# Optimization experiments

Measured on AMD Instinct MI355X. Metric: run time of the kernel, lower is better.

## Reference

```python
import jax, jax.numpy as jnp
import numpy as np

D_MODEL = 256
H = 4              # hardcoded in the torch module via repeat(1,4,1)
DIM = D_MODEL // H # 64
N = 4096


def _conv1x1(x, W, b):
    # torch Conv1d(kernel_size=1): [B, Cin, N] -> [B, Cout, N]
    return jnp.einsum('oi,bin->bon', W, x) + b[None, :, None]


def setup_inputs() -> dict:
    key = jax.random.key(0)
    ks = jax.random.split(key, 13)
    s = 0.02
    inp = {
        'query':   jax.random.normal(ks[0], (1, D_MODEL, N), dtype=jnp.float32),
        'key':     jax.random.normal(ks[1], (1, D_MODEL, N), dtype=jnp.float32),
        'value':   jax.random.normal(ks[2], (1, D_MODEL, N), dtype=jnp.float32),
        'coords0': jax.random.normal(ks[3], (1, 3, N), dtype=jnp.float32),
        'coords1': jax.random.normal(ks[4], (1, 3, N), dtype=jnp.float32),
        'Wq': jax.random.normal(ks[5], (D_MODEL, D_MODEL), dtype=jnp.float32) * s,
        'bq': jnp.zeros((D_MODEL,), dtype=jnp.float32),
        'Wk': jax.random.normal(ks[6], (D_MODEL, D_MODEL), dtype=jnp.float32) * s,
        'bk': jnp.zeros((D_MODEL,), dtype=jnp.float32),
        'Wv': jax.random.normal(ks[7], (D_MODEL, D_MODEL), dtype=jnp.float32) * s,
        'bv': jnp.zeros((D_MODEL,), dtype=jnp.float32),
        'Wm': jax.random.normal(ks[8], (D_MODEL + 28, D_MODEL + 28), dtype=jnp.float32) * s,
        'bm': jnp.zeros((D_MODEL + 28,), dtype=jnp.float32),
    }
    return inp


def reference(query, key, value, coords0, coords1, Wq, bq, Wk, bk, Wv, bv, Wm, bm):
    B = query.shape[0]  # must be 1 (hardcoded in original via view(1,4,3,-1))
    Nq = coords0.shape[2]
    Nk = coords1.shape[2]

    # 1x1-conv projections, then split channels into (dim, heads): view(B, dim, H, N)
    q = _conv1x1(query, Wq, bq).reshape(B, DIM, H, Nq)
    k = _conv1x1(key,   Wk, bk).reshape(B, DIM, H, Nk)
    v = _conv1x1(value, Wv, bv).reshape(B, DIM, H, Nk)

    # coords1.repeat(1,4,1).view(1,4,3,-1).transpose(1,2) == broadcast coords over heads
    c1 = jnp.broadcast_to(coords1[:, :, None, :], (B, 3, H, Nk))
    v = jnp.concatenate([v, c1], axis=1)  # [B, DIM+3, H, Nk]

    # attention: scale is query.shape[1]**0.5 == DIM**0.5 (per-head dim)
    scores = jnp.einsum('bdhn,bdhm->bhnm', q, k) / jnp.asarray(DIM, q.dtype) ** 0.5
    prob = jax.nn.softmax(scores, axis=-1)          # [B, H, Nq, Nk]
    x = jnp.einsum('bhnm,bdhm->bdhn', prob, v)      # [B, DIM+3, H, Nq]

    # coordinate augmentation
    c0 = jnp.broadcast_to(coords0[:, :, None, :], (B, 3, H, Nq))
    aug1 = x[:, DIM:DIM + 3] - c0                   # [B, 3, H, Nq]
    aug2 = jnp.linalg.norm(aug1, axis=1, keepdims=True)  # [B, 1, H, Nq]

    y = jnp.concatenate([x, aug1, aug2], axis=1)    # [B, DIM+7, H, Nq]
    y = y.reshape(B, (DIM + 7) * H, Nq)
    return _conv1x1(y, Wm, bm)                      # [B, d_model+28, Nq]
```

## Files before the change

### kernel.cpp

```cpp
#include <hip/hip_runtime.h>
#include <hip/hip_bf16.h>

#define NN 4096

typedef __attribute__((ext_vector_type(8))) short short8;
typedef __attribute__((ext_vector_type(4))) float f32x4;

__device__ __forceinline__ unsigned short f2bf(float f) {
  union { float f; unsigned u; } v; v.f = f;
  unsigned u = v.u;
  u += 0x7fffu + ((u >> 16) & 1u);
  return (unsigned short)(u >> 16);
}

__device__ __forceinline__ unsigned packpair(float a, float b) {
  __hip_bfloat162 h = __float22bfloat162_rn(make_float2(a, b));
  union { __hip_bfloat162 h; unsigned u; } cv; cv.h = h;
  return cv.u;
}

__device__ __forceinline__ float bf2f(unsigned short us) {
  union { unsigned u; float f; } cv; cv.u = (unsigned)us << 16;
  return cv.f;
}

__global__ __launch_bounds__(256) void transpose3_kernel(
    const float* __restrict__ q, const float* __restrict__ k, const float* __restrict__ v,
    unsigned short* __restrict__ Xt, const float* __restrict__ coords1,
    unsigned short* __restrict__ Vb) {
  __shared__ float Tl[64][65];
  const float* X = (blockIdx.z == 0) ? q : (blockIdx.z == 1) ? k : v;
  unsigned short* dst = Xt + (size_t)blockIdx.z * NN * 256;
  const int n0 = blockIdx.x << 6, k0 = blockIdx.y << 6;
  const int t = threadIdx.x;
  const int r = t >> 4, c4 = (t & 15) << 2;
#pragma unroll
  for (int i = 0; i < 4; ++i) {
    const float4 vv = *(const float4*)(X + (size_t)(k0 + r + 16 * i) * NN + n0 + c4);
    Tl[r + 16 * i][c4] = vv.x; Tl[r + 16 * i][c4 + 1] = vv.y;
    Tl[r + 16 * i][c4 + 2] = vv.z; Tl[r + 16 * i][c4 + 3] = vv.w;
  }
  __syncthreads();
  const int kc = (t & 7) << 3;
#pragma unroll
  for (int j = 0; j < 2; ++j) {
    const int n = (t >> 3) + (j << 5);
    unsigned pk[4];
#pragma unroll
    for (int u = 0; u < 4; ++u)
      pk[u] = packpair(Tl[kc + 2 * u][n], Tl[kc + 2 * u + 1][n]);
    *(uint4*)(dst + (size_t)(n0 + n) * 256 + k0 + kc) = *(uint4*)pk;
  }
  if (blockIdx.z == 2 && blockIdx.y == 0) {
    const int rr = t >> 2, seg = t & 3;
    const int h = rr >> 4, d = 64 + (rr & 15);
    unsigned short* vd = Vb + (size_t)(h * 80 + d) * NN + n0 + seg * 16;
    if (d < 67) {
      const float* src = coords1 + (size_t)(d - 64) * NN + n0 + seg * 16;
      unsigned u[8];
#pragma unroll
      for (int i = 0; i < 4; ++i) {
        const float4 cv = *(const float4*)(src + 4 * i);
        u[2 * i] = packpair(cv.x, cv.y);
        u[2 * i + 1] = packpair(cv.z, cv.w);
      }
      *(uint4*)vd = *(uint4*)&u[0];
      *(uint4*)(vd + 8) = *(uint4*)&u[4];
    } else {
      const uint4 zz = make_uint4(0u, 0u, 0u, 0u);
      *(uint4*)vd = zz;
      *(uint4*)(vd + 8) = zz;
    }
  }
}

__global__ __launch_bounds__(256) void proj_gemm_kernel(
    const float* __restrict__ Wq, const float* __restrict__ bq,
    const float* __restrict__ Wk, const float* __restrict__ bk,
    const float* __restrict__ Wv, const float* __restrict__ bv,
    const unsigned short* __restrict__ Xt,
    unsigned short* __restrict__ Qb, unsigned short* __restrict__ Kb,
    unsigned short* __restrict__ Vb) {
  __shared__ __align__(16) unsigned char smem[16384];
  __shared__ float Bls[64];
  const int z = blockIdx.z;
  const float* W  = (z == 0) ? Wq : (z == 1) ? Wk : Wv;
  const float* bb = (z == 0) ? bq : (z == 1) ? bk : bv;
  const unsigned short* Xz = Xt + (size_t)z * NN * 256;
  const int co0 = blockIdx.y << 6;
  const int n0 = blockIdx.x << 6;
  const int tid = threadIdx.x;
  const int w = tid >> 6, l = tid & 63;
  const int wm = w >> 1, wn = w & 1;
  const int c = l & 15, g = l >> 4;
  char* const Al = (char*)smem;
  char* const Bl = (char*)smem + 8192;

  if (tid < 64) Bls[tid] = bb[co0 + tid];

  const int ar = tid >> 2, ac = (tid & 3) << 4;
  const int br = tid >> 3, bch = tid & 7;
  const int aswz = (ar & 7) << 4;
  const int bswz = (br & 7) << 4;

  float4 wa[4];
  uint4 wb[2];
  f32x4 acc[2][2];
#pragma unroll
  for (int mf = 0; mf < 2; ++mf)
#pragma unroll
    for (int nf = 0; nf < 2; ++nf) acc[mf][nf] = (f32x4){0.f, 0.f, 0.f, 0.f};

#define PJ_LOAD(k0_) do { \
  _Pragma("unroll") for (int i = 0; i < 4; ++i) \
    wa[i] = *(const float4*)(W + (size_t)(co0 + ar) * 256 + (k0_) + ac + 4 * i); \
  wb[0] = *(const uint4*)(Xz + (size_t)(n0 + br) * 256 + (k0_) + bch * 8); \
  wb[1] = *(const uint4*)(Xz + (size_t)(n0 + br + 32) * 256 + (k0_) + bch * 8); \
} while (0)

#define PJ_STORE() do { \
  unsigned pk[8]; \
  _Pragma("unroll") for (int i = 0; i < 4; ++i) { \
    pk[2 * i] = packpair(wa[i].x, wa[i].y); \
    pk[2 * i + 1] = packpair(wa[i].z, wa[i].w); \
  } \
  *(uint4*)(Al + ar * 128 + (((ac << 1)) ^ aswz)) = *(uint4*)&pk[0]; \
  *(uint4*)(Al + ar * 128 + (((ac << 1) + 16) ^ aswz)) = *(uint4*)&pk[4]; \
  *(uint4*)(Bl + br * 128 + ((bch << 4) ^ bswz)) = wb[0]; \
  *(uint4*)(Bl + (br + 32) * 128 + ((bch << 4) ^ bswz)) = wb[1]; \
} while (0)

  PJ_LOAD(0);
  PJ_STORE();
  __syncthreads();

  for (int s = 0; s < 4; ++s) {
    const bool hav = (s + 1 < 4);
    if (hav) PJ_LOAD((s + 1) << 6);
    __builtin_amdgcn_s_setprio(1);
#pragma unroll
    for (int ks = 0; ks < 2; ++ks) {
      short8 af[2], bf[2];
#pragma unroll
      for (int mf = 0; mf < 2; ++mf) {
        const int row = wm * 32 + mf * 16 + c;
        af[mf] = *(const short8*)(Al + row * 128 + (((ks << 6) + (g << 4)) ^ ((row & 7) << 4)));
      }
#pragma unroll
      for (int nf = 0; nf < 2; ++nf) {
        const int row = wn * 32 + nf * 16 + c;
        bf[nf] = *(const short8*)(Bl + row * 128 + (((ks << 6) + (g << 4)) ^ ((row & 7) << 4)));
      }
#pragma unroll
      for (int mf = 0; mf < 2; ++mf)
#pragma unroll
        for (int nf = 0; nf < 2; ++nf)
          acc[mf][nf] = __builtin_amdgcn_mfma_f32_16x16x32_bf16(af[mf], bf[nf], acc[mf][nf], 0, 0, 0);
    }
    __builtin_amdgcn_s_setprio(0);
    __syncthreads();
    if (hav) {
      PJ_STORE();
      __syncthreads();
    }
  }

  unsigned short* Clu = (unsigned short*)smem;
  const float scale = (z == 0) ? 0.18033688f : 1.0f;
#pragma unroll
  for (int mf = 0; mf < 2; ++mf)
#pragma unroll
    for (int nf = 0; nf < 2; ++nf)
#pragma unroll
      for (int rr = 0; rr < 4; ++rr) {
        const int row = wm * 32 + mf * 16 + (g << 2) + rr;
        const int col = wn * 32 + nf * 16 + c;
        Clu[row * 72 + col] = f2bf((acc[mf][nf][rr] + Bls[row]) * scale);
      }
  __syncthreads();
  if (z <= 1) {
    unsigned short* Ob = (z == 0) ? Qb : Kb;
    const int d0 = co0 >> 2;
    const int h = tid >> 6, n = tid & 63;
    unsigned u[8];
#pragma unroll
    for (int p = 0; p < 8; ++p)
      u[p] = (unsigned)Clu[((p << 3) + h) * 72 + n] |
             ((unsigned)Clu[((p << 3) + 4 + h) * 72 + n] << 16);
    uint4* dd = (uint4*)(Ob + ((size_t)h * NN + n0 + n) * 64 + d0);
    dd[0] = *(uint4*)&u[0];
    dd[1] = *(uint4*)&u[4];
  } else {
    const int rl = tid >> 2, seg = (tid & 3) << 4;
    const int h = rl & 3, d = (co0 >> 2) + (rl >> 2);
    unsigned short* vd = Vb + (size_t)(h * 80 + d) * NN + n0 + seg;
    *(uint4*)vd = *(const uint4*)((char*)Clu + rl * 144 + (seg << 1));
    *(uint4*)(vd + 8) = *(const uint4*)((char*)Clu + rl * 144 + (seg << 1) + 16);
  }
}

__global__ __launch_bounds__(256, 2) void attn_kernel(
    const unsigned short* __restrict__ Qb, const unsigned short* __restrict__ Kb,
    const unsigned short* __restrict__ Vb, unsigned short* __restrict__ ObT,
    float* __restrict__ Ml, int chunkKeys, int nsplit) {
  __shared__ __align__(16) unsigned char smem[71680];
  const int b = blockIdx.x;
  int x, h, sp;
  if (nsplit >= 2) {
    const int xcd = b & 7, slot = b >> 3;
    const int group = xcd * (nsplit >> 1) + (slot >> 5);
    x = slot & 31; h = group & 3; sp = group >> 2;
  } else {
    x = b & 31; h = (b >> 5) & 3; sp = 0;
  }
  const int qbase = x * 128;
  const int tid = threadIdx.x;
  const int w = tid >> 6;
  const int l = tid & 63;
  const int c = l & 15;
  const int g = l >> 4;
  const int swc = (c & 7) << 4;

  char* const Pls = (char*)smem + 55296 + w * 4096;

  short8 qf[2][2];
#pragma unroll
  for (int qs = 0; qs < 2; ++qs) {
    const unsigned short* qsrc = Qb + (((h * NN) + qbase + w * 32 + qs * 16 + c) << 6) + (g << 3);
    qf[qs][0] = *(const short8*)qsrc;
    qf[qs][1] = *(const short8*)(qsrc + 32);
  }

  f32x4 Of[2][5];
#pragma unroll
  for (int qs = 0; qs < 2; ++qs)
#pragma unroll
    for (int dt = 0; dt < 5; ++dt) Of[qs][dt] = (f32x4){0.f, 0.f, 0.f, 0.f};
  float mrun[2] = {-1e30f, -1e30f};
  float lrun[2] = {0.f, 0.f};

  const int r0 = tid >> 3, ch = tid & 7;
  const int so = (ch << 4) ^ ((r0 & 7) << 4);
  const int mStart = sp * chunkKeys;
  const int niter = chunkKeys >> 6;

  uint4 ska, skb, sva, svb, svc;

#define LOADT(m0_) do { \
    const unsigned short* kbase_ = Kb + ((h * NN + (m0_)) << 6); \
    const unsigned short* vbase_ = Vb + (size_t)(h * 80) * NN + (m0_); \
    ska = *(const uint4*)(kbase_ + (r0 << 6) + (ch << 3)); \
    skb = *(const uint4*)(kbase_ + ((r0 + 32) << 6) + (ch << 3)); \
    sva = *(const uint4*)(vbase_ + (size_t)r0 * NN + (ch << 3)); \
    svb = *(const uint4*)(vbase_ + (size_t)(r0 + 32) * NN + (ch << 3)); \
    if (tid < 128) svc = *(const uint4*)(vbase_ + (size_t)(r0 + 64) * NN + (ch << 3)); \
  } while (0)

#define STORET(bj_) do { \
    char* Kd_ = (char*)smem + (bj_) * 18432; \
    char* Vd_ = Kd_ + 8192; \
    *(uint4*)(Kd_ + r0 * 128 + so) = ska; \
    *(uint4*)(Kd_ + (r0 + 32) * 128 + so) = skb; \
    *(uint4*)(Vd_ + r0 * 128 + so) = sva; \
    *(uint4*)(Vd_ + (r0 + 32) * 128 + so) = svb; \
    if (tid < 128) *(uint4*)(Vd_ + (r0 + 64) * 128 + so) = svc; \
  } while (0)

#define QKSTEP(bj_, DST) do { \
    const char* Kc_ = (char*)smem + (bj_) * 18432; \
    __builtin_amdgcn_s_setprio(1); \
    _Pragma("unroll") for (int t = 0; t < 4; ++t) { \
      const char* rp_ = Kc_ + (t * 16 + c) * 128; \
      const short8 k0_ = *(const short8*)(rp_ + ((g << 4) ^ swc)); \
      const short8 k1_ = *(const short8*)(rp_ + ((64 + (g << 4)) ^ swc)); \
      _Pragma("unroll") for (int qs = 0; qs < 2; ++qs) { \
        f32x4 a_ = (f32x4){0.f, 0.f, 0.f, 0.f}; \
        a_ = __builtin_amdgcn_mfma_f32_16x16x32_bf16(k0_, qf[qs][0], a_, 0, 0, 0); \
        a_ = __builtin_amdgcn_mfma_f32_16x16x32_bf16(k1_, qf[qs][1], a_, 0, 0, 0); \
        DST[qs][t] = a_; \
      } \
    } \
    __builtin_amdgcn_s_setprio(0); \
  } while (0)

#define SMSTEP(SRC) do { \
    _Pragma("unroll") for (int qs = 0; qs < 2; ++qs) { \
      float m01_ = fmaxf(fmaxf(SRC[qs][0][0], SRC[qs][0][1]), fmaxf(SRC[qs][0][2], SRC[qs][0][3])); \
      float m11_ = fmaxf(fmaxf(SRC[qs][1][0], SRC[qs][1][1]), fmaxf(SRC[qs][1][2], SRC[qs][1][3])); \
      float m21_ = fmaxf(fmaxf(SRC[qs][2][0], SRC[qs][2][1]), fmaxf(SRC[qs][2][2], SRC[qs][2][3])); \
      float m31_ = fmaxf(fmaxf(SRC[qs][3][0], SRC[qs][3][1]), fmaxf(SRC[qs][3][2], SRC[qs][3][3])); \
      float mx_ = fmaxf(fmaxf(m01_, m11_), fmaxf(m21_, m31_)); \
      mx_ = fmaxf(mx_, __shfl_xor(mx_, 16)); \
      mx_ = fmaxf(mx_, __shfl_xor(mx_, 32)); \
      if (!__all(mx_ - mrun[qs] <= 11.5f)) { \
        const float mn_ = fmaxf(mrun[qs], mx_); \
        const float a_ = __builtin_amdgcn_exp2f(mrun[qs] - mn_); \
        mrun[qs] = mn_; \
        lrun[qs] *= a_; \
        _Pragma("unroll") for (int dt = 0; dt < 5; ++dt) \
          _Pragma("unroll") for (int r = 0; r < 4; ++r) Of[qs][dt][r] *= a_; \
      } \
      const float mm_ = mrun[qs]; \
      float rs_ = 0.f; \
      unsigned pk_[8]; \
      _Pragma("unroll") for (int t = 0; t < 4; ++t) { \
        const float e0_ = __builtin_amdgcn_exp2f(SRC[qs][t][0] - mm_); \
        const float e1_ = __builtin_amdgcn_exp2f(SRC[qs][t][1] - mm_); \
        const float e2_ = __builtin_amdgcn_exp2f(SRC[qs][t][2] - mm_); \
        const float e3_ = __builtin_amdgcn_exp2f(SRC[qs][t][3] - mm_); \
        rs_ += (e0_ + e1_) + (e2_ + e3_); \
        pk_[t * 2]     = packpair(e0_, e1_); \
        pk_[t * 2 + 1] = packpair(e2_, e3_); \
      } \
      rs_ += __shfl_xor(rs_, 16); \
      rs_ += __shfl_xor(rs_, 32); \
      lrun[qs] += rs_; \
      char* prow_ = Pls + (qs * 16 + c) * 128; \
      _Pragma("unroll") for (int t = 0; t < 4; ++t) \
        *(uint2*)(prow_ + ((t * 32 + (g << 3)) ^ swc)) = make_uint2(pk_[t * 2], pk_[t * 2 + 1]); \
    } \
  } while (0)

#define PVSTEP(bj_) do { \
    short8 pb_[2][2]; \
    _Pragma("unroll") for (int qs = 0; qs < 2; ++qs) { \
      const char* prow_ = Pls + (qs * 16 + c) * 128; \
      pb_[qs][0] = *(const short8*)(prow_ + ((g << 4) ^ swc)); \
      pb_[qs][1] = *(const short8*)(prow_ + ((64 + (g << 4)) ^ swc)); \
    } \
    const char* Vc_ = (char*)smem + (bj_) * 18432 + 8192; \
    __builtin_amdgcn_s_setprio(1); \
    _Pragma("unroll") for (int dt = 0; dt < 5; ++dt) { \
      const char* vp_ = Vc_ + (dt * 16 + c) * 128; \
      const short8 v0_ = *(const short8*)(vp_ + ((g << 4) ^ swc)); \
      const short8 v1_ = *(const short8*)(vp_ + ((64 + (g << 4)) ^ swc)); \
      _Pragma("unroll") for (int qs = 0; qs < 2; ++qs) { \
        Of[qs][dt] = __builtin_amdgcn_mfma_f32_16x16x32_bf16(v0_, pb_[qs][0], Of[qs][dt], 0, 0, 0); \
        Of[qs][dt] = __builtin_amdgcn_mfma_f32_16x16x32_bf16(v1_, pb_[qs][1], Of[qs][dt], 0, 0, 0); \
      } \
    } \
    __builtin_amdgcn_s_setprio(0); \
  } while (0)

  f32x4 sD0[2][4], sD1[2][4];

  LOADT(mStart);
  STORET(0);
  LOADT(mStart + 64);
  __syncthreads();
  QKSTEP(0, sD0);
  STORET(1);
  LOADT(mStart + 128);
  __syncthreads();

  for (int it = 0; it < niter; it += 2) {
    SMSTEP(sD0);
    QKSTEP((it + 1) % 3, sD1);
    PVSTEP(it % 3);
    if (it + 2 < niter) {
      STORET((it + 2) % 3);
      if (it + 3 < niter) LOADT(mStart + ((it + 3) << 6));
    }
    __syncthreads();
    SMSTEP(sD1);
    if (it + 2 < niter) QKSTEP((it + 2) % 3, sD0);
    PVSTEP((it + 1) % 3);
    if (it + 3 < niter) {
      STORET((it + 3) % 3);
      if (it + 4 < niter) LOADT(mStart + ((it + 4) << 6));
    }
    __syncthreads();
  }

#undef LOADT
#undef STORET
#undef QKSTEP
#undef SMSTEP
#undef PVSTEP

  const int hb = sp * 4 + h;
#pragma unroll
  for (int qs = 0; qs < 2; ++qs) {
    const int qg = qbase + w * 32 + qs * 16 + c;
    unsigned short* orow = ObT + ((size_t)hb * NN + qg) * 72;
#pragma unroll
    for (int dt = 0; dt < 5; ++dt) {
      if (dt == 4 && g >= 2) continue;
      const unsigned lo = packpair(Of[qs][dt][0], Of[qs][dt][1]);
      const unsigned hi = packpair(Of[qs][dt][2], Of[qs][dt][3]);
      *(uint2*)(orow + dt * 16 + (g << 2)) = make_uint2(lo, hi);
    }
    if (g == 0) {
      Ml[((size_t)hb * 2 + 0) * NN + qg] = mrun[qs];
      Ml[((size_t)hb * 2 + 1) * NN + qg] = lrun[qs];
    }
  }
}

template <int NS>
__global__ __launch_bounds__(256) void combine_t_kernel(
    const unsigned short* __restrict__ ObT, const float* __restrict__ Ml,
    const float* __restrict__ coords0, unsigned short* __restrict__ Yt) {
  __shared__ __align__(16) unsigned char Yl[16 * 640];
  const int t = threadIdx.x;
  const int q = t & 15;
  const int worker = t >> 4;
  const int h = worker & 3;
  const int dgrp = worker >> 2;
  const int q0 = blockIdx.x << 4;
  const int qg = q0 + q;
  const int rowb = q * 640;
  const int sw = (q & 7) << 4;

  float m[NS], wgt[NS], lv[NS];
#pragma unroll
  for (int s = 0; s < NS; ++s)
    m[s] = Ml[((size_t)(s * 4 + h) * 2 + 0) * NN + qg];
#pragma unroll
  for (int s = 0; s < NS; ++s)
    lv[s] = Ml[((size_t)(s * 4 + h) * 2 + 1) * NN + qg];
  float M = -1e30f;
#pragma unroll
  for (int s = 0; s < NS; ++s) M = fmaxf(M, m[s]);
  float L = 0.f;
#pragma unroll
  for (int s = 0; s < NS; ++s) {
    wgt[s] = __builtin_amdgcn_exp2f(m[s] - M);
    L += lv[s] * wgt[s];
  }
  const float invL = 1.f / L;
#pragma unroll
  for (int s = 0; s < NS; ++s) wgt[s] *= invL;

  if (worker == 0) *(uint2*)(Yl + rowb + (568 ^ sw)) = make_uint2(0u, 0u);

  const int c0 = dgrp << 4;
  const int nch = (dgrp == 3) ? 3 : 2;
  uint4 ld[NS][3];
#pragma unroll
  for (int s = 0; s < NS; ++s) {
    const unsigned short* orow = ObT + ((size_t)(s * 4 + h) * NN + qg) * 72 + c0;
#pragma unroll
    for (int i = 0; i < 3; ++i)
      if (i < nch) ld[s][i] = *(const uint4*)(orow + (i << 3));
  }

  float ss = 0.f;
#pragma unroll
  for (int i = 0; i < 3; ++i) {
    if (i < nch) {
#pragma unroll
      for (int e = 0; e < 8; ++e) {
        const int dv = c0 + (i << 3) + e;
        if (dv < 67) {
          float a = 0.f;
#pragma unroll
          for (int s = 0; s < NS; ++s) {
            const unsigned short us = ((const unsigned short*)&ld[s][i])[e];
            a = fmaf(bf2f(us), wgt[s], a);
          }
          *(unsigned short*)(Yl + rowb + ((((dv << 2) + h) << 1) ^ sw)) = f2bf(a);
          if (dv >= 64) {
            const float au = a - coords0[(size_t)(dv - 64) * NN + qg];
            *(unsigned short*)(Yl + rowb + (((((dv + 3) << 2) + h) << 1) ^ sw)) = f2bf(au);
            ss += au * au;
          }
        }
      }
    }
  }
  if (dgrp == 3) *(unsigned short*)(Yl + rowb + (((280 + h) << 1) ^ sw)) = f2bf(sqrtf(ss));
  __syncthreads();

  for (int i = t; i < 16 * 36; i += 256) {
    const int row = i / 36, seg = i - row * 36;
    *(uint4*)(Yt + (size_t)(q0 + row) * 288 + (seg << 3)) =
        *(const uint4*)(Yl + row * 640 + ((seg << 4) ^ ((row & 7) << 4)));
  }
}

#define OP_LOAD(k0_) do { \
  const int arow = co0 + ar; \
  _Pragma("unroll") for (int i = 0; i < 6; ++i) { \
    const int col = (k0_) + ac + 4 * i; \
    wa[i] = (arow < 284 && col < 284) ? *(const float4*)(Wm + (size_t)arow * 284 + col) \
                                      : make_float4(0.f, 0.f, 0.f, 0.f); \
  } \
  _Pragma("unroll") for (int i = 0; i < 3; ++i) \
    wb[i] = *(const uint4*)(Yt + (size_t)(n0 + bn) * 288 + (k0_) + bc + 8 * i); \
} while (0)

#define OP_WRITE_LDS() do { \
  unsigned pk[12]; \
  _Pragma("unroll") for (int i = 0; i < 6; ++i) { \
    pk[2 * i] = packpair(wa[i].x, wa[i].y); \
    pk[2 * i + 1] = packpair(wa[i].z, wa[i].w); \
  } \
  _Pragma("unroll") for (int i = 0; i < 3; ++i) \
    *(uint4*)(Al + ar * 256 + (((ac << 1) + (i << 4)) ^ aswz)) = *(uint4*)&pk[4 * i]; \
  _Pragma("unroll") for (int i = 0; i < 3; ++i) \
    *(uint4*)(Bl + bn * 256 + (((bc << 1) + (i << 4)) ^ bswz)) = wb[i]; \
} while (0)

__global__ __launch_bounds__(256) void outproj_gemm_kernel(
    const unsigned short* __restrict__ Yt, const float* __restrict__ Wm,
    const float* __restrict__ bm, float* __restrict__ out) {
  __shared__ __align__(16) unsigned char smem[32768];
  __shared__ float Bls[64];
  const int co0 = blockIdx.y << 6;
  const int n0 = blockIdx.x << 6;
  const int tid = threadIdx.x;
  const int w = tid >> 6, l = tid & 63;
  const int wm = w >> 1, wn = w & 1;
  const int c = l & 15, g = l >> 4;
  char* const Al = (char*)smem;
  char* const Bl = (char*)smem + 16384;

  if (tid < 64) { const int co = co0 + tid; Bls[tid] = (co < 284) ? bm[co] : 0.f; }

  const int ar = tid >> 2, ac = (tid & 3) * 24;
  const int bn = tid >> 2, bc = (tid & 3) * 24;
  const int aswz = (ar & 7) << 4;
  const int bswz = (bn & 7) << 4;

  float4 wa[6];
  uint4 wb[3];
  f32x4 acc[2][2];
#pragma unroll
  for (int mf = 0; mf < 2; ++mf)
#pragma unroll
    for (int nf = 0; nf < 2; ++nf) acc[mf][nf] = (f32x4){0.f, 0.f, 0.f, 0.f};

  OP_LOAD(0);
  OP_WRITE_LDS();
  __syncthreads();

  for (int s = 0; s < 3; ++s) {
    const bool hav = (s + 1 < 3);
    if (hav) OP_LOAD((s + 1) * 96);
    __builtin_amdgcn_s_setprio(1);
#pragma unroll
    for (int ks = 0; ks < 3; ++ks) {
      short8 af[2], bf[2];
#pragma unroll
      for (int mf = 0; mf < 2; ++mf) {
        const int row = wm * 32 + mf * 16 + c;
        af[mf] = *(const short8*)(Al + row * 256 + (((ks << 6) + (g << 4)) ^ ((row & 7) << 4)));
      }
#pragma unroll
      for (int nf = 0; nf < 2; ++nf) {
        const int row = wn * 32 + nf * 16 + c;
        bf[nf] = *(const short8*)(Bl + row * 256 + (((ks << 6) + (g << 4)) ^ ((row & 7) << 4)));
      }
#pragma unroll
      for (int mf = 0; mf < 2; ++mf)
#pragma unroll
        for (int nf = 0; nf < 2; ++nf)
          acc[mf][nf] = __builtin_amdgcn_mfma_f32_16x16x32_bf16(af[mf], bf[nf], acc[mf][nf], 0, 0, 0);
    }
    __builtin_amdgcn_s_setprio(0);
    __syncthreads();
    if (hav) {
      OP_WRITE_LDS();
      __syncthreads();
    }
  }

#pragma unroll
  for (int mf = 0; mf < 2; ++mf)
#pragma unroll
    for (int nf = 0; nf < 2; ++nf)
#pragma unroll
      for (int rr = 0; rr < 4; ++rr) {
        const int row = wm * 32 + mf * 16 + (g << 2) + rr;
        const int co = co0 + row;
        if (co < 284)
          out[(size_t)co * NN + n0 + wn * 32 + nf * 16 + c] = acc[mf][nf][rr] + Bls[row];
      }
}

extern "C" void kernel_launch(void* const* d_in, const int* in_sizes, int n_in,
                              void* d_out, int out_size, void* d_ws, size_t ws_size,
                              hipStream_t stream) {
  const float* query   = (const float*)d_in[0];
  const float* key_    = (const float*)d_in[1];
  const float* value   = (const float*)d_in[2];
  const float* coords0 = (const float*)d_in[3];
  const float* coords1 = (const float*)d_in[4];
  const float* Wq = (const float*)d_in[5];
  const float* bq = (const float*)d_in[6];
  const float* Wk = (const float*)d_in[7];
  const float* bk = (const float*)d_in[8];
  const float* Wv = (const float*)d_in[9];
  const float* bv = (const float*)d_in[10];
  const float* Wm = (const float*)d_in[11];
  const float* bm = (const float*)d_in[12];
  float* out = (float*)d_out;

  unsigned short* Qb = (unsigned short*)d_ws;
  unsigned short* Kb = Qb + (size_t)4 * NN * 64;
  unsigned short* Vb = Kb + (size_t)4 * NN * 64;
  unsigned short* Xt = Vb + (size_t)4 * 80 * NN;
  unsigned short* Yt = Xt + (size_t)3 * NN * 256;
  unsigned short* ObT = Yt + (size_t)NN * 288;

  const size_t fixedB = (size_t)((char*)ObT - (char*)d_ws);
  const size_t per = (size_t)4 * NN * 72 * 2 + (size_t)4 * 2 * NN * 4;
  int nsplit = 4;
  while (nsplit > 1 && ws_size < fixedB + (size_t)nsplit * per) nsplit >>= 1;
  float* Ml = (float*)(ObT + (size_t)nsplit * 4 * NN * 72);

  hipLaunchKernelGGL(transpose3_kernel, dim3(64, 4, 3), dim3(256), 0, stream,
                     query, key_, value, Xt, coords1, Vb);
  hipLaunchKernelGGL(proj_gemm_kernel, dim3(64, 4, 3), dim3(256), 0, stream,
                     Wq, bq, Wk, bk, Wv, bv, Xt, Qb, Kb, Vb);
  hipLaunchKernelGGL(attn_kernel, dim3(128 * nsplit), dim3(256), 0, stream,
                     Qb, Kb, Vb, ObT, Ml, NN / nsplit, nsplit);
  switch (nsplit) {
    case 4:
      hipLaunchKernelGGL((combine_t_kernel<4>), dim3(256), dim3(256), 0, stream, ObT, Ml, coords0, Yt);
      break;
    case 2:
      hipLaunchKernelGGL((combine_t_kernel<2>), dim3(256), dim3(256), 0, stream, ObT, Ml, coords0, Yt);
      break;
    default:
      hipLaunchKernelGGL((combine_t_kernel<1>), dim3(256), dim3(256), 0, stream, ObT, Ml, coords0, Yt);
      break;
  }
  hipLaunchKernelGGL(outproj_gemm_kernel, dim3(64, 5), dim3(256), 0, stream, Yt, Wm, bm, out);
}
```

Baseline: 75.84 us.

## Software-pipeline softmax of next tile against PV MFMA of current tile

Restructures the flash-attention inner loop so each iteration computes QK scores for tile it+1, reads the stored P fragments for tile it, runs the exp/softmax for tile it+1, and then issues the PV MFMAs for tile it. The running-max rescale of the output accumulators is deferred until after the PV MFMAs and applied through a flag and a stored factor. The aim is to let the exp VALU work overlap MFMA execution and to reduce register pressure by keeping a single score buffer instead of two. In exchange, the loop is no longer unrolled by two, so the modulo-3 buffer indexing is computed every iteration and there is a separate epilogue for the last tile.

```diff
diff --git a/kernel.cpp b/kernel.cpp
--- a/kernel.cpp
+++ b/kernel.cpp
@@ -238,6 +238,8 @@
     for (int dt = 0; dt < 5; ++dt) Of[qs][dt] = (f32x4){0.f, 0.f, 0.f, 0.f};
   float mrun[2] = {-1e30f, -1e30f};
   float lrun[2] = {0.f, 0.f};
+  float alv[2] = {1.f, 1.f};
+  bool resc[2] = {false, false};
 
   const int r0 = tid >> 3, ch = tid & 7;
   const int so = (ch << 4) ^ ((r0 & 7) << 4);
@@ -245,6 +247,8 @@
   const int niter = chunkKeys >> 6;
 
   uint4 ska, skb, sva, svb, svc;
+  short8 pb[2][2];
+  f32x4 sD[2][4];
 
 #define LOADT(m0_) do { \
     const unsigned short* kbase_ = Kb + ((h * NN + (m0_)) << 6); \
@@ -266,7 +270,7 @@
     if (tid < 128) *(uint4*)(Vd_ + (r0 + 64) * 128 + so) = svc; \
   } while (0)
 
-#define QKSTEP(bj_, DST) do { \
+#define QKSTEP(bj_) do { \
     const char* Kc_ = (char*)smem + (bj_) * 18432; \
     __builtin_amdgcn_s_setprio(1); \
     _Pragma("unroll") for (int t = 0; t < 4; ++t) { \
@@ -277,37 +281,46 @@
         f32x4 a_ = (f32x4){0.f, 0.f, 0.f, 0.f}; \
         a_ = __builtin_amdgcn_mfma_f32_16x16x32_bf16(k0_, qf[qs][0], a_, 0, 0, 0); \
         a_ = __builtin_amdgcn_mfma_f32_16x16x32_bf16(k1_, qf[qs][1], a_, 0, 0, 0); \
-        DST[qs][t] = a_; \
+        sD[qs][t] = a_; \
       } \
     } \
     __builtin_amdgcn_s_setprio(0); \
   } while (0)
 
-#define SMSTEP(SRC) do { \
+#define PBREAD() do { \
     _Pragma("unroll") for (int qs = 0; qs < 2; ++qs) { \
-      float m01_ = fmaxf(fmaxf(SRC[qs][0][0], SRC[qs][0][1]), fmaxf(SRC[qs][0][2], SRC[qs][0][3])); \
-      float m11_ = fmaxf(fmaxf(SRC[qs][1][0], SRC[qs][1][1]), fmaxf(SRC[qs][1][2], SRC[qs][1][3])); \
-      float m21_ = fmaxf(fmaxf(SRC[qs][2][0], SRC[qs][2][1]), fmaxf(SRC[qs][2][2], SRC[qs][2][3])); \
-      float m31_ = fmaxf(fmaxf(SRC[qs][3][0], SRC[qs][3][1]), fmaxf(SRC[qs][3][2], SRC[qs][3][3])); \
+      const char* prow_ = Pls + (qs * 16 + c) * 128; \
+      pb[qs][0] = *(const short8*)(prow_ + ((g << 4) ^ swc)); \
+      pb[qs][1] = *(const short8*)(prow_ + ((64 + (g << 4)) ^ swc)); \
+    } \
+  } while (0)
+
+#define SM_EXP() do { \
+    _Pragma("unroll") for (int qs = 0; qs < 2; ++qs) { \
+      float m01_ = fmaxf(fmaxf(sD[qs][0][0], sD[qs][0][1]), fmaxf(sD[qs][0][2], sD[qs][0][3])); \
+      float m11_ = fmaxf(fmaxf(sD[qs][1][0], sD[qs][1][1]), fmaxf(sD[qs][1][2], sD[qs][1][3])); \
+      float m21_ = fmaxf(fmaxf(sD[qs][2][0], sD[qs][2][1]), fmaxf(sD[qs][2][2], sD[qs][2][3])); \
+      float m31_ = fmaxf(fmaxf(sD[qs][3][0], sD[qs][3][1]), fmaxf(sD[qs][3][2], sD[qs][3][3])); \
       float mx_ = fmaxf(fmaxf(m01_, m11_), fmaxf(m21_, m31_)); \
       mx_ = fmaxf(mx_, __shfl_xor(mx_, 16)); \
       mx_ = fmaxf(mx_, __shfl_xor(mx_, 32)); \
       if (!__all(mx_ - mrun[qs] <= 11.5f)) { \
         const float mn_ = fmaxf(mrun[qs], mx_); \
-        const float a_ = __builtin_amdgcn_exp2f(mrun[qs] - mn_); \
+        alv[qs] = __builtin_amdgcn_exp2f(mrun[qs] - mn_); \
         mrun[qs] = mn_; \
-        lrun[qs] *= a_; \
-        _Pragma("unroll") for (int dt = 0; dt < 5; ++dt) \
-          _Pragma("unroll") for (int r = 0; r < 4; ++r) Of[qs][dt][r] *= a_; \
+        lrun[qs] *= alv[qs]; \
+        resc[qs] = true; \
+      } else { \
+        resc[qs] = false; \
       } \
       const float mm_ = mrun[qs]; \
       float rs_ = 0.f; \
       unsigned pk_[8]; \
       _Pragma("unroll") for (int t = 0; t < 4; ++t) { \
-        const float e0_ = __builtin_amdgcn_exp2f(SRC[qs][t][0] - mm_); \
-        const float e1_ = __builtin_amdgcn_exp2f(SRC[qs][t][1] - mm_); \
-        const float e2_ = __builtin_amdgcn_exp2f(SRC[qs][t][2] - mm_); \
-        const float e3_ = __builtin_amdgcn_exp2f(SRC[qs][t][3] - mm_); \
+        const float e0_ = __builtin_amdgcn_exp2f(sD[qs][t][0] - mm_); \
+        const float e1_ = __builtin_amdgcn_exp2f(sD[qs][t][1] - mm_); \
+        const float e2_ = __builtin_amdgcn_exp2f(sD[qs][t][2] - mm_); \
+        const float e3_ = __builtin_amdgcn_exp2f(sD[qs][t][3] - mm_); \
         rs_ += (e0_ + e1_) + (e2_ + e3_); \
         pk_[t * 2]     = packpair(e0_, e1_); \
         pk_[t * 2 + 1] = packpair(e2_, e3_); \
@@ -321,13 +334,7 @@
     } \
   } while (0)
 
-#define PVSTEP(bj_) do { \
-    short8 pb_[2][2]; \
-    _Pragma("unroll") for (int qs = 0; qs < 2; ++qs) { \
-      const char* prow_ = Pls + (qs * 16 + c) * 128; \
-      pb_[qs][0] = *(const short8*)(prow_ + ((g << 4) ^ swc)); \
-      pb_[qs][1] = *(const short8*)(prow_ + ((64 + (g << 4)) ^ swc)); \
-    } \
+#define PVMM(bj_) do { \
     const char* Vc_ = (char*)smem + (bj_) * 18432 + 8192; \
     __builtin_amdgcn_s_setprio(1); \
     _Pragma("unroll") for (int dt = 0; dt < 5; ++dt) { \
@@ -335,48 +342,53 @@
       const short8 v0_ = *(const short8*)(vp_ + ((g << 4) ^ swc)); \
       const short8 v1_ = *(const short8*)(vp_ + ((64 + (g << 4)) ^ swc)); \
       _Pragma("unroll") for (int qs = 0; qs < 2; ++qs) { \
-        Of[qs][dt] = __builtin_amdgcn_mfma_f32_16x16x32_bf16(v0_, pb_[qs][0], Of[qs][dt], 0, 0, 0); \
-        Of[qs][dt] = __builtin_amdgcn_mfma_f32_16x16x32_bf16(v1_, pb_[qs][1], Of[qs][dt], 0, 0, 0); \
+        Of[qs][dt] = __builtin_amdgcn_mfma_f32_16x16x32_bf16(v0_, pb[qs][0], Of[qs][dt], 0, 0, 0); \
+        Of[qs][dt] = __builtin_amdgcn_mfma_f32_16x16x32_bf16(v1_, pb[qs][1], Of[qs][dt], 0, 0, 0); \
       } \
     } \
     __builtin_amdgcn_s_setprio(0); \
   } while (0)
 
-  f32x4 sD0[2][4], sD1[2][4];
+#define OF_RESCALE() do { \
+    _Pragma("unroll") for (int qs = 0; qs < 2; ++qs) \
+      if (resc[qs]) { \
+        _Pragma("unroll") for (int dt = 0; dt < 5; ++dt) \
+          _Pragma("unroll") for (int r = 0; r < 4; ++r) Of[qs][dt][r] *= alv[qs]; \
+      } \
+  } while (0)
 
   LOADT(mStart);
   STORET(0);
   LOADT(mStart + 64);
   __syncthreads();
-  QKSTEP(0, sD0);
+  QKSTEP(0);
   STORET(1);
   LOADT(mStart + 128);
   __syncthreads();
-
-  for (int it = 0; it < niter; it += 2) {
-    SMSTEP(sD0);
-    QKSTEP((it + 1) % 3, sD1);
-    PVSTEP(it % 3);
+  SM_EXP();
+
+  for (int it = 0; it < niter - 1; ++it) {
+    QKSTEP((it + 1) % 3);
+    PBREAD();
+    SM_EXP();
+    PVMM(it % 3);
+    OF_RESCALE();
     if (it + 2 < niter) {
       STORET((it + 2) % 3);
       if (it + 3 < niter) LOADT(mStart + ((it + 3) << 6));
     }
     __syncthreads();
-    SMSTEP(sD1);
-    if (it + 2 < niter) QKSTEP((it + 2) % 3, sD0);
-    PVSTEP((it + 1) % 3);
-    if (it + 3 < niter) {
-      STORET((it + 3) % 3);
-      if (it + 4 < niter) LOADT(mStart + ((it + 4) << 6));
-    }
-    __syncthreads();
-  }
+  }
+  PBREAD();
+  PVMM((niter - 1) % 3);
 
 #undef LOADT
 #undef STORET
 #undef QKSTEP
-#undef SMSTEP
-#undef PVSTEP
+#undef PBREAD
+#undef SM_EXP
+#undef PVMM
+#undef OF_RESCALE
 
   const int hb = sp * 4 + h;
 #pragma unroll
```

New measurement: 76.84 us, median of 2. About the same (+1.3%).
